# Performance work log

Measured on AMD Instinct MI355X. Metric: run time of the kernel, lower is better.

Reference implementation:

```python
import jax, jax.numpy as jnp
import numpy as np

N_POINTS = 1048576
N_CLUSTERS = 16384
D_FEAT = 64


def setup_inputs() -> dict:
    key = jax.random.key(0)
    ks = jax.random.split(key, 6)
    features = jax.random.normal(ks[0], (N_CLUSTERS, D_FEAT), dtype=jnp.float32)
    labels = jax.random.randint(ks[1], (N_POINTS,), 0, N_CLUSTERS, dtype=jnp.int32)
    cluster_centers = jax.random.normal(ks[2], (N_CLUSTERS, 3), dtype=jnp.float32)
    points = jax.random.normal(ks[3], (N_POINTS, 3), dtype=jnp.float32)
    # Glorot-uniform like Keras Dense defaults
    lim1 = np.sqrt(6.0 / (D_FEAT + 3 + 128)).astype(np.float32)
    lim2 = np.sqrt(6.0 / (128 + 64)).astype(np.float32)
    W1 = jax.random.uniform(ks[4], (D_FEAT + 3, 128), minval=-lim1, maxval=lim1, dtype=jnp.float32)
    b1 = jnp.zeros((128,), dtype=jnp.float32)
    W2 = jax.random.uniform(ks[5], (128, 64), minval=-lim2, maxval=lim2, dtype=jnp.float32)
    b2 = jnp.zeros((64,), dtype=jnp.float32)
    return {"features": features, "labels": labels, "cluster_centers": cluster_centers,
            "points": points, "W1": W1, "b1": b1, "W2": W2, "b2": b2}


def reference(features, labels, cluster_centers, points, W1, b1, W2, b2):
    center_features = features[labels]                 # [N, D_FEAT] gather
    point_center_coords = cluster_centers[labels]      # [N, 3] gather
    x = jnp.concatenate([center_features, point_center_coords - points], axis=-1)  # [N, 67]
    h = jax.nn.relu(x @ W1 + b1)                       # [N, 128]
    out = jax.nn.relu(h @ W2 + b2)                     # [N, 64]
    return out
```

## Files before the change

kernel.cpp:

```cpp
#include <hip/hip_runtime.h>
#include <hip/hip_bf16.h>

#define NPTS 1048576
#define NCLU 16384
#define DF   64
#define H1   128
#define H2   64
#define BP   64
#define NBLK 1024
#define ITERS (NPTS / (BP * NBLK))
#define K1P  104
#define K2P  136

typedef __bf16 bf16x8 __attribute__((ext_vector_type(8)));
typedef float  f32x4  __attribute__((ext_vector_type(4)));
typedef unsigned short u16x4 __attribute__((ext_vector_type(4)));
typedef unsigned short u16x8 __attribute__((ext_vector_type(8)));

__device__ __forceinline__ unsigned short f2b(float f) {
  unsigned v; __builtin_memcpy(&v, &f, 4);
  v += 0x7fffu + ((v >> 16) & 1u);
  return (unsigned short)(v >> 16);
}

__global__ __launch_bounds__(256, 4)
void cvt_feat(const float* __restrict__ f, unsigned short* __restrict__ o) {
  int i = (blockIdx.x * 256 + threadIdx.x) * 4;
  f32x4 v = *(const f32x4*)&f[i];
  u16x4 h;
  #pragma unroll
  for (int j = 0; j < 4; ++j) h[j] = f2b(v[j]);
  *(u16x4*)&o[i] = h;
}

__global__ __launch_bounds__(256, 2)
void fused_gather_mlp(const float* __restrict__ feat,
                      const int* __restrict__ labels,
                      const float* __restrict__ centers,
                      const float* __restrict__ points,
                      const float* __restrict__ W1,
                      const float* __restrict__ b1,
                      const float* __restrict__ W2,
                      const float* __restrict__ b2,
                      float* __restrict__ out,
                      const unsigned short* __restrict__ featbf,
                      int use_bf)
{
  __shared__ __align__(16) unsigned short sX[BP][K1P];
  __shared__ __align__(16) unsigned short sW1[H1][K1P];
  __shared__ __align__(16) unsigned short sH[BP][K2P];
  __shared__ __align__(16) unsigned short sW2[H2][K2P];
  __shared__ __align__(16) float sB1[H1];
  __shared__ __align__(16) float sB2[H2];

  const int t    = threadIdx.x;
  const int w    = t >> 6;
  const int lane = t & 63;
  const int quad = lane >> 4, l16 = lane & 15;
  const int m0   = w * 16;

  if (t < 32)            *(f32x4*)&sB1[t * 4]        = *(const f32x4*)&b1[t * 4];
  else if (t < 48)       *(f32x4*)&sB2[(t - 32) * 4] = *(const f32x4*)&b2[(t - 32) * 4];

  #pragma unroll
  for (int i = 0; i < 6; ++i) {
    int task = t + 256 * i;
    int n = task & 127, kc = task >> 7;
    u16x8 h;
    #pragma unroll
    for (int j = 0; j < 8; ++j) {
      int k = kc * 8 + j;
      float v = (k < 67) ? W1[k * H1 + n] : 0.f;
      h[j] = f2b(v);
    }
    *(u16x8*)&sW1[n][kc * 8] = h;
  }
  #pragma unroll
  for (int i = 0; i < 4; ++i) {
    int task = t + 256 * i;
    int n = task & 63, kc = task >> 6;
    u16x8 h;
    #pragma unroll
    for (int j = 0; j < 8; ++j) h[j] = f2b(W2[(kc * 8 + j) * H2 + n]);
    *(u16x8*)&sW2[n][kc * 8] = h;
  }
  if (lane < 48) {
    int r = lane & 15, c = 9 + (lane >> 4);
    u16x8 z = {0, 0, 0, 0, 0, 0, 0, 0};
    *(u16x8*)&sX[m0 + r][c * 8] = z;
  }
  __syncthreads();

  float bias1[8], bias2[4];
  #pragma unroll
  for (int nt = 0; nt < 8; ++nt) bias1[nt] = sB1[nt * 16 + l16];
  #pragma unroll
  for (int nt = 0; nt < 4; ++nt) bias2[nt] = sB2[nt * 16 + l16];

  for (int it = 0; it < ITERS; ++it) {
    const int p0 = (blockIdx.x * ITERS + it) * BP;

    #pragma unroll
    for (int i = 0; i < 2; ++i) {
      int task = lane + 64 * i;
      int row = task >> 3, kc = task & 7;
      int lab = labels[p0 + m0 + row];
      if (use_bf) {
        *(u16x8*)&sX[m0 + row][kc * 8] = *(const u16x8*)&featbf[lab * DF + kc * 8];
      } else {
        f32x4 v0 = *(const f32x4*)&feat[lab * DF + kc * 8];
        f32x4 v1 = *(const f32x4*)&feat[lab * DF + kc * 8 + 4];
        u16x8 h;
        #pragma unroll
        for (int j = 0; j < 4; ++j) { h[j] = f2b(v0[j]); h[j + 4] = f2b(v1[j]); }
        *(u16x8*)&sX[m0 + row][kc * 8] = h;
      }
    }
    if (lane < 16) {
      int row = lane, p = p0 + m0 + row;
      int lab = labels[p];
      u16x8 h = {0, 0, 0, 0, 0, 0, 0, 0};
      #pragma unroll
      for (int j = 0; j < 3; ++j) h[j] = f2b(centers[lab * 3 + j] - points[p * 3 + j]);
      *(u16x8*)&sX[m0 + row][DF] = h;
    }

    f32x4 acc[8];
    #pragma unroll
    for (int i = 0; i < 8; ++i) acc[i] = (f32x4){0.f, 0.f, 0.f, 0.f};
    #pragma unroll
    for (int ks = 0; ks < 3; ++ks) {
      int k0 = ks * 32 + quad * 8;
      bf16x8 a = *(const bf16x8*)&sX[m0 + l16][k0];
      #pragma unroll
      for (int nt = 0; nt < 8; ++nt) {
        bf16x8 b = *(const bf16x8*)&sW1[nt * 16 + l16][k0];
        acc[nt] = __builtin_amdgcn_mfma_f32_16x16x32_bf16(a, b, acc[nt], 0, 0, 0);
      }
    }
    #pragma unroll
    for (int nt = 0; nt < 8; ++nt) {
      int n = nt * 16 + l16;
      #pragma unroll
      for (int r = 0; r < 4; ++r) {
        float v = acc[nt][r] + bias1[nt];
        v = v > 0.f ? v : 0.f;
        sH[m0 + quad * 4 + r][n] = f2b(v);
      }
    }

    f32x4 acc2[4];
    #pragma unroll
    for (int i = 0; i < 4; ++i) acc2[i] = (f32x4){0.f, 0.f, 0.f, 0.f};
    #pragma unroll
    for (int ks = 0; ks < 4; ++ks) {
      int k0 = ks * 32 + quad * 8;
      bf16x8 a = *(const bf16x8*)&sH[m0 + l16][k0];
      #pragma unroll
      for (int nt = 0; nt < 4; ++nt) {
        bf16x8 b = *(const bf16x8*)&sW2[nt * 16 + l16][k0];
        acc2[nt] = __builtin_amdgcn_mfma_f32_16x16x32_bf16(a, b, acc2[nt], 0, 0, 0);
      }
    }
    #pragma unroll
    for (int nt = 0; nt < 4; ++nt) {
      int n = nt * 16 + l16;
      #pragma unroll
      for (int r = 0; r < 4; ++r) {
        float v = acc2[nt][r] + bias2[nt];
        v = v > 0.f ? v : 0.f;
        out[(long)(p0 + m0 + quad * 4 + r) * H2 + n] = v;
      }
    }
  }
}

extern "C" void kernel_launch(void* const* d_in, const int* in_sizes, int n_in,
                              void* d_out, int out_size, void* d_ws, size_t ws_size,
                              hipStream_t stream) {
  const float* feat   = (const float*)d_in[0];
  const int*   labels = (const int*)d_in[1];
  const float* cen    = (const float*)d_in[2];
  const float* pts    = (const float*)d_in[3];
  const float* W1     = (const float*)d_in[4];
  const float* b1     = (const float*)d_in[5];
  const float* W2     = (const float*)d_in[6];
  const float* b2     = (const float*)d_in[7];
  float*       outp   = (float*)d_out;

  const size_t featbf_bytes = (size_t)NCLU * DF * sizeof(unsigned short);
  int use_bf = (ws_size >= featbf_bytes) ? 1 : 0;
  unsigned short* featbf = (unsigned short*)d_ws;

  if (use_bf)
    cvt_feat<<<dim3(NCLU * DF / (256 * 4)), dim3(256), 0, stream>>>(feat, featbf);

  fused_gather_mlp<<<dim3(NBLK), dim3(256), 0, stream>>>(
      feat, labels, cen, pts, W1, b1, W2, b2, outp, featbf, use_bf);
}
```

Before: 383.7 us.

## Compute transposed MFMA tiles with register-resident A operands and W2, fold biases

Swaps the MFMA operand roles so each lane holds its own point's gathered features directly in registers, removing the sX staging buffer. Bias1 is folded into W1 as an extra input row fed by a constant 1. W2 fragments and bias2 now live in registers, which frees LDS and lets occupancy rise to 3 blocks per SIMD with a 768-block grid-stride loop. Output is written as contiguous float4 per lane, replacing scattered scalar stores. The cost is more register pressure from the W2 fragments, which may spill or limit occupancy.

```diff
diff --git a/kernel.cpp b/kernel.cpp
--- a/kernel.cpp
+++ b/kernel.cpp
@@ -7,12 +7,13 @@
 #define H1   128
 #define H2   64
 #define BP   64
-#define NBLK 1024
-#define ITERS (NPTS / (BP * NBLK))
+#define NBLK 768
+#define NTILES (NPTS / BP)
 #define K1P  104
 #define K2P  136
 
 typedef __bf16 bf16x8 __attribute__((ext_vector_type(8)));
+typedef __bf16 bf16x4 __attribute__((ext_vector_type(4)));
 typedef float  f32x4  __attribute__((ext_vector_type(4)));
 typedef unsigned short u16x4 __attribute__((ext_vector_type(4)));
 typedef unsigned short u16x8 __attribute__((ext_vector_type(8)));
@@ -33,7 +34,7 @@
   *(u16x4*)&o[i] = h;
 }
 
-__global__ __launch_bounds__(256, 2)
+__global__ __launch_bounds__(256, 3)
 void fused_gather_mlp(const float* __restrict__ feat,
                       const int* __restrict__ labels,
                       const float* __restrict__ centers,
@@ -46,21 +47,14 @@
                       const unsigned short* __restrict__ featbf,
                       int use_bf)
 {
-  __shared__ __align__(16) unsigned short sX[BP][K1P];
   __shared__ __align__(16) unsigned short sW1[H1][K1P];
   __shared__ __align__(16) unsigned short sH[BP][K2P];
-  __shared__ __align__(16) unsigned short sW2[H2][K2P];
-  __shared__ __align__(16) float sB1[H1];
-  __shared__ __align__(16) float sB2[H2];
 
   const int t    = threadIdx.x;
   const int w    = t >> 6;
   const int lane = t & 63;
   const int quad = lane >> 4, l16 = lane & 15;
   const int m0   = w * 16;
-
-  if (t < 32)            *(f32x4*)&sB1[t * 4]        = *(const f32x4*)&b1[t * 4];
-  else if (t < 48)       *(f32x4*)&sB2[(t - 32) * 4] = *(const f32x4*)&b2[(t - 32) * 4];
 
   #pragma unroll
   for (int i = 0; i < 6; ++i) {
@@ -70,107 +64,99 @@
     #pragma unroll
     for (int j = 0; j < 8; ++j) {
       int k = kc * 8 + j;
-      float v = (k < 67) ? W1[k * H1 + n] : 0.f;
+      float v = (k < 67) ? W1[k * H1 + n] : ((k == 67) ? b1[n] : 0.f);
       h[j] = f2b(v);
     }
     *(u16x8*)&sW1[n][kc * 8] = h;
   }
+
+  bf16x8 w2f[4][4];
   #pragma unroll
-  for (int i = 0; i < 4; ++i) {
-    int task = t + 256 * i;
-    int n = task & 63, kc = task >> 6;
-    u16x8 h;
+  for (int nt2 = 0; nt2 < 4; ++nt2) {
     #pragma unroll
-    for (int j = 0; j < 8; ++j) h[j] = f2b(W2[(kc * 8 + j) * H2 + n]);
-    *(u16x8*)&sW2[n][kc * 8] = h;
+    for (int ks = 0; ks < 4; ++ks) {
+      #pragma unroll
+      for (int j = 0; j < 8; ++j)
+        w2f[nt2][ks][j] = (__bf16)W2[(ks * 32 + quad * 8 + j) * H2 + (nt2 * 16 + l16)];
+    }
   }
-  if (lane < 48) {
-    int r = lane & 15, c = 9 + (lane >> 4);
-    u16x8 z = {0, 0, 0, 0, 0, 0, 0, 0};
-    *(u16x8*)&sX[m0 + r][c * 8] = z;
-  }
+  f32x4 bias2v[4];
+  #pragma unroll
+  for (int nt2 = 0; nt2 < 4; ++nt2)
+    bias2v[nt2] = *(const f32x4*)&b2[nt2 * 16 + quad * 4];
+
   __syncthreads();
 
-  float bias1[8], bias2[4];
-  #pragma unroll
-  for (int nt = 0; nt < 8; ++nt) bias1[nt] = sB1[nt * 16 + l16];
-  #pragma unroll
-  for (int nt = 0; nt < 4; ++nt) bias2[nt] = sB2[nt * 16 + l16];
+  for (int tile = blockIdx.x; tile < NTILES; tile += NBLK) {
+    const int p0  = tile * BP;
+    const int p   = p0 + m0 + l16;
+    const int lab = labels[p];
 
-  for (int it = 0; it < ITERS; ++it) {
-    const int p0 = (blockIdx.x * ITERS + it) * BP;
-
-    #pragma unroll
-    for (int i = 0; i < 2; ++i) {
-      int task = lane + 64 * i;
-      int row = task >> 3, kc = task & 7;
-      int lab = labels[p0 + m0 + row];
-      if (use_bf) {
-        *(u16x8*)&sX[m0 + row][kc * 8] = *(const u16x8*)&featbf[lab * DF + kc * 8];
-      } else {
-        f32x4 v0 = *(const f32x4*)&feat[lab * DF + kc * 8];
-        f32x4 v1 = *(const f32x4*)&feat[lab * DF + kc * 8 + 4];
-        u16x8 h;
-        #pragma unroll
-        for (int j = 0; j < 4; ++j) { h[j] = f2b(v0[j]); h[j + 4] = f2b(v1[j]); }
-        *(u16x8*)&sX[m0 + row][kc * 8] = h;
+    bf16x8 ax0, ax1;
+    if (use_bf) {
+      ax0 = *(const bf16x8*)&featbf[(long)lab * DF + quad * 8];
+      ax1 = *(const bf16x8*)&featbf[(long)lab * DF + 32 + quad * 8];
+    } else {
+      f32x4 v0 = *(const f32x4*)&feat[(long)lab * DF + quad * 8];
+      f32x4 v1 = *(const f32x4*)&feat[(long)lab * DF + quad * 8 + 4];
+      f32x4 v2 = *(const f32x4*)&feat[(long)lab * DF + 32 + quad * 8];
+      f32x4 v3 = *(const f32x4*)&feat[(long)lab * DF + 32 + quad * 8 + 4];
+      #pragma unroll
+      for (int j = 0; j < 4; ++j) {
+        ax0[j] = (__bf16)v0[j]; ax0[j + 4] = (__bf16)v1[j];
+        ax1[j] = (__bf16)v2[j]; ax1[j + 4] = (__bf16)v3[j];
       }
     }
-    if (lane < 16) {
-      int row = lane, p = p0 + m0 + row;
-      int lab = labels[p];
-      u16x8 h = {0, 0, 0, 0, 0, 0, 0, 0};
-      #pragma unroll
-      for (int j = 0; j < 3; ++j) h[j] = f2b(centers[lab * 3 + j] - points[p * 3 + j]);
-      *(u16x8*)&sX[m0 + row][DF] = h;
+    bf16x8 a2;
+    #pragma unroll
+    for (int j = 0; j < 8; ++j) a2[j] = (__bf16)0.0f;
+    if (quad == 0) {
+      float d0 = centers[lab * 3 + 0] - points[(long)p * 3 + 0];
+      float d1 = centers[lab * 3 + 1] - points[(long)p * 3 + 1];
+      float d2 = centers[lab * 3 + 2] - points[(long)p * 3 + 2];
+      a2[0] = (__bf16)d0; a2[1] = (__bf16)d1; a2[2] = (__bf16)d2;
+      a2[3] = (__bf16)1.0f;
     }
 
-    f32x4 acc[8];
+    f32x4 acc1[8];
     #pragma unroll
-    for (int i = 0; i < 8; ++i) acc[i] = (f32x4){0.f, 0.f, 0.f, 0.f};
+    for (int i = 0; i < 8; ++i) acc1[i] = (f32x4){0.f, 0.f, 0.f, 0.f};
     #pragma unroll
-    for (int ks = 0; ks < 3; ++ks) {
-      int k0 = ks * 32 + quad * 8;
-      bf16x8 a = *(const bf16x8*)&sX[m0 + l16][k0];
-      #pragma unroll
-      for (int nt = 0; nt < 8; ++nt) {
-        bf16x8 b = *(const bf16x8*)&sW1[nt * 16 + l16][k0];
-        acc[nt] = __builtin_amdgcn_mfma_f32_16x16x32_bf16(a, b, acc[nt], 0, 0, 0);
-      }
+    for (int nt = 0; nt < 8; ++nt) {
+      bf16x8 wa = *(const bf16x8*)&sW1[nt * 16 + l16][quad * 8];
+      bf16x8 wb = *(const bf16x8*)&sW1[nt * 16 + l16][32 + quad * 8];
+      bf16x8 wc = *(const bf16x8*)&sW1[nt * 16 + l16][64 + quad * 8];
+      acc1[nt] = __builtin_amdgcn_mfma_f32_16x16x32_bf16(wa, ax0, acc1[nt], 0, 0, 0);
+      acc1[nt] = __builtin_amdgcn_mfma_f32_16x16x32_bf16(wb, ax1, acc1[nt], 0, 0, 0);
+      acc1[nt] = __builtin_amdgcn_mfma_f32_16x16x32_bf16(wc, a2,  acc1[nt], 0, 0, 0);
     }
     #pragma unroll
     for (int nt = 0; nt < 8; ++nt) {
-      int n = nt * 16 + l16;
+      bf16x4 hv;
       #pragma unroll
       for (int r = 0; r < 4; ++r) {
-        float v = acc[nt][r] + bias1[nt];
-        v = v > 0.f ? v : 0.f;
-        sH[m0 + quad * 4 + r][n] = f2b(v);
+        float v = acc1[nt][r];
+        hv[r] = (__bf16)(v > 0.f ? v : 0.f);
       }
+      *(bf16x4*)&sH[m0 + l16][nt * 16 + quad * 4] = hv;
     }
 
     f32x4 acc2[4];
     #pragma unroll
-    for (int i = 0; i < 4; ++i) acc2[i] = (f32x4){0.f, 0.f, 0.f, 0.f};
+    for (int i = 0; i < 4; ++i) acc2[i] = bias2v[i];
     #pragma unroll
     for (int ks = 0; ks < 4; ++ks) {
-      int k0 = ks * 32 + quad * 8;
-      bf16x8 a = *(const bf16x8*)&sH[m0 + l16][k0];
+      bf16x8 hf = *(const bf16x8*)&sH[m0 + l16][ks * 32 + quad * 8];
       #pragma unroll
-      for (int nt = 0; nt < 4; ++nt) {
-        bf16x8 b = *(const bf16x8*)&sW2[nt * 16 + l16][k0];
-        acc2[nt] = __builtin_amdgcn_mfma_f32_16x16x32_bf16(a, b, acc2[nt], 0, 0, 0);
-      }
+      for (int nt2 = 0; nt2 < 4; ++nt2)
+        acc2[nt2] = __builtin_amdgcn_mfma_f32_16x16x32_bf16(w2f[nt2][ks], hf, acc2[nt2], 0, 0, 0);
     }
     #pragma unroll
-    for (int nt = 0; nt < 4; ++nt) {
-      int n = nt * 16 + l16;
+    for (int nt2 = 0; nt2 < 4; ++nt2) {
+      f32x4 v = acc2[nt2];
       #pragma unroll
-      for (int r = 0; r < 4; ++r) {
-        float v = acc2[nt][r] + bias2[nt];
-        v = v > 0.f ? v : 0.f;
-        out[(long)(p0 + m0 + quad * 4 + r) * H2 + n] = v;
-      }
+      for (int r = 0; r < 4; ++r) v[r] = v[r] > 0.f ? v[r] : 0.f;
+      *(f32x4*)&out[(long)p * H2 + nt2 * 16 + quad * 4] = v;
     }
   }
 }
```

After: 466.2 us. +21.5%, slower.
